# Performance work log

Hardware: AMD Instinct MI355X
Metric: run time of the kernel (lower is better)

## Reference

```python
import jax, jax.numpy as jnp
import numpy as np
from jax import lax

K = 16  # number of KNN neighbors (fixed in module)


def _knn_neighbors(x, k):
    # x: (B, 3, N) point coordinates -> neighbor coords (B, 3, N, K)
    inner = jnp.einsum('bdn,bdm->bnm', x, x)          # (B, N, N)
    sq = jnp.sum(x * x, axis=1)                        # (B, N)
    d2 = sq[:, :, None] + sq[:, None, :] - 2.0 * inner  # pairwise sq dists (B, N, N)
    _, nbr_idx = lax.top_k(-d2, k)                     # k nearest (incl. self), (B, N, K)
    # gather neighbor coordinates: expand x to (B, 3, 1, N), idx to (B, 1, N, K)
    neighbor = jnp.take_along_axis(x[:, :, None, :], nbr_idx[:, None, :, :], axis=3)
    return neighbor  # (B, 3, N, K)


def _down_index(neighbor, x, npts_ds):
    # center-diff saliency: sum of squared offsets to K neighbors per point
    diff = neighbor - x[:, :, :, None]                 # (B, 3, N, K)
    score = jnp.sum(diff * diff, axis=(1, 3))          # (B, N)
    _, idx = lax.top_k(score, npts_ds)                 # (B, npts_ds)
    return idx


def setup_inputs() -> dict:
    key = jax.random.key(0)
    k1, k2 = jax.random.split(key)
    B, N, C = 8, 4096, 128
    x = jax.random.normal(k1, (B, 3, N), dtype=jnp.float32)
    y = jax.random.normal(k2, (B, C, N), dtype=jnp.float32)
    return {"x": x, "y": y, "npts_ds": 2048}


def reference(x, y, npts_ds):
    B, _, N = x.shape
    C = y.shape[1]
    neighbor = _knn_neighbors(x, K)                    # ops.group(x, K, 'neighbor')
    idx = _down_index(neighbor, x, npts_ds)            # ops.down_index(...), (B, npts_ds)
    idx3 = jnp.broadcast_to(idx[:, None, :], (B, 3, npts_ds))
    idxC = jnp.broadcast_to(idx[:, None, :], (B, C, npts_ds))
    top_k_xyz = jnp.take_along_axis(x, idx3, axis=2)    # (B, 3, npts_ds)
    top_k_points = jnp.take_along_axis(y, idxC, axis=2)  # (B, C, npts_ds)
    return (top_k_xyz, top_k_points)
```

## Files before the change

kernel.cpp:

```cpp
#include <hip/hip_runtime.h>
#include <math.h>

#define BATCH 8
#define NPTS 4096
#define CHAN 128
#define KNN 16
#define SPLIT 4
#define CHUNK (NPTS / SPLIT)
#define ISPLIT 2
#define QCH (CHUNK / ISPLIT)
#define EPC 24
#define RSPLIT 4
#define RCHUNK (NPTS / RSPLIT)

typedef unsigned long long u64;

__device__ __forceinline__ u64 pack_key(float d2, int idx) {
  unsigned b = __float_as_uint(d2);
  b ^= (unsigned)((int)b >> 31) | 0x80000000u;
  return ((u64)b << 32) | (unsigned)idx;
}

__device__ __forceinline__ float d2_ref(float4 q, float ppx, float ppy,
                                        float ppz, float psq) {
  float inner = __fadd_rn(__fadd_rn(__fmul_rn(ppx, q.x), __fmul_rn(ppy, q.y)),
                          __fmul_rn(ppz, q.z));
  return __fsub_rn(__fadd_rn(psq, q.w), __fmul_rn(2.0f, inner));
}

__device__ __forceinline__ void ce_asc(u64& x, u64& y) {
  bool sw = y < x;
  u64 lo = sw ? y : x;
  u64 hi = sw ? x : y;
  x = lo;
  y = hi;
}

__device__ __forceinline__ void batcher_sort16_u64(u64 a[16]) {
#define CE(i, j) ce_asc(a[i], a[j])
  CE(0, 8); CE(1, 9); CE(2, 10); CE(3, 11);
  CE(4, 12); CE(5, 13); CE(6, 14); CE(7, 15);
  CE(0, 4); CE(1, 5); CE(2, 6); CE(3, 7);
  CE(8, 12); CE(9, 13); CE(10, 14); CE(11, 15);
  CE(4, 8); CE(5, 9); CE(6, 10); CE(7, 11);
  CE(0, 2); CE(1, 3); CE(4, 6); CE(5, 7);
  CE(8, 10); CE(9, 11); CE(12, 14); CE(13, 15);
  CE(2, 8); CE(3, 9); CE(6, 12); CE(7, 13);
  CE(2, 4); CE(3, 5); CE(6, 8); CE(7, 9); CE(10, 12); CE(11, 13);
  CE(0, 1); CE(2, 3); CE(4, 5); CE(6, 7);
  CE(8, 9); CE(10, 11); CE(12, 13); CE(14, 15);
  CE(1, 8); CE(3, 10); CE(5, 12); CE(7, 14);
  CE(1, 4); CE(3, 6); CE(5, 8); CE(7, 10); CE(9, 12); CE(11, 14);
  CE(1, 2); CE(3, 4); CE(5, 6); CE(7, 8); CE(9, 10); CE(11, 12); CE(13, 14);
#undef CE
}

__device__ __forceinline__ void bitonic_sort32(u64 a[32]) {
#pragma unroll
  for (int k = 2; k <= 32; k <<= 1) {
#pragma unroll
    for (int j = k >> 1; j > 0; j >>= 1) {
#pragma unroll
      for (int i = 0; i < 32; ++i) {
        int l = i ^ j;
        if (l > i) {
          if ((i & k) == 0) ce_asc(a[i], a[l]);
          else              ce_asc(a[l], a[i]);
        }
      }
    }
  }
}

__device__ __forceinline__ void merge_keep16(u64 T[16], const u64 A[16]) {
  u64 nt[16];
#pragma unroll
  for (int i = 0; i < 16; ++i) {
    u64 a = A[15 - i];
    nt[i] = (a < T[i]) ? a : T[i];
  }
#pragma unroll
  for (int j = 8; j > 0; j >>= 1) {
#pragma unroll
    for (int i = 0; i < 16; ++i) {
      int l = i ^ j;
      if (l > i) ce_asc(nt[i], nt[l]);
    }
  }
#pragma unroll
  for (int i = 0; i < 16; ++i) T[i] = nt[i];
}

__device__ __forceinline__ void ce_i32(int& x, int& y) {
  int lo = (x < y) ? x : y;
  int hi = (x < y) ? y : x;
  x = lo;
  y = hi;
}

__device__ __forceinline__ void batcher_sort16_i32(int a[16]) {
#define CE(i, j) ce_i32(a[i], a[j])
  CE(0, 8); CE(1, 9); CE(2, 10); CE(3, 11);
  CE(4, 12); CE(5, 13); CE(6, 14); CE(7, 15);
  CE(0, 4); CE(1, 5); CE(2, 6); CE(3, 7);
  CE(8, 12); CE(9, 13); CE(10, 14); CE(11, 15);
  CE(4, 8); CE(5, 9); CE(6, 10); CE(7, 11);
  CE(0, 2); CE(1, 3); CE(4, 6); CE(5, 7);
  CE(8, 10); CE(9, 11); CE(12, 14); CE(13, 15);
  CE(2, 8); CE(3, 9); CE(6, 12); CE(7, 13);
  CE(2, 4); CE(3, 5); CE(6, 8); CE(7, 9); CE(10, 12); CE(11, 13);
  CE(0, 1); CE(2, 3); CE(4, 5); CE(6, 7);
  CE(8, 9); CE(10, 11); CE(12, 13); CE(14, 15);
  CE(1, 8); CE(3, 10); CE(5, 12); CE(7, 14);
  CE(1, 4); CE(3, 6); CE(5, 8); CE(7, 10); CE(9, 12); CE(11, 14);
  CE(1, 2); CE(3, 4); CE(5, 6); CE(7, 8); CE(9, 10); CE(11, 12); CE(13, 14);
#undef CE
}

__device__ __forceinline__ void merge_keep16_i32(int T[16], const int A[16]) {
  int nt[16];
#pragma unroll
  for (int i = 0; i < 16; ++i) {
    int a = A[15 - i];
    nt[i] = (a < T[i]) ? a : T[i];
  }
#pragma unroll
  for (int j = 8; j > 0; j >>= 1) {
#pragma unroll
    for (int i = 0; i < 16; ++i) {
      int l = i ^ j;
      if (l > i) ce_i32(nt[i], nt[l]);
    }
  }
#pragma unroll
  for (int i = 0; i < 16; ++i) T[i] = nt[i];
}

__global__ __attribute__((amdgpu_waves_per_eu(4, 4)))
__launch_bounds__(512) void knn_partial_kernel(
    const float* __restrict__ x, u64* __restrict__ pkey) {
  const int s = blockIdx.x % SPLIT;
  const int ntile = (blockIdx.x / SPLIT) % (NPTS / 256);
  const int b = blockIdx.x / (SPLIT * (NPTS / 256));
  const int p = threadIdx.x & 255;
  const int h = threadIdx.x >> 8;
  __shared__ float4 xs[CHUNK];
  __shared__ unsigned short ebuf[512 * EPC];
  __shared__ u64 mbuf[KNN][256];

  const float* xb = x + (size_t)b * 3 * NPTS;
  for (int i = threadIdx.x; i < CHUNK; i += 512) {
    int gm = s * CHUNK + i;
    float px = xb[gm];
    float py = xb[NPTS + gm];
    float pz = xb[2 * NPTS + gm];
    float sq = __fadd_rn(__fadd_rn(__fmul_rn(px, px), __fmul_rn(py, py)),
                         __fmul_rn(pz, pz));
    xs[i] = make_float4(px, py, pz, sq);
  }

  const int n = ntile * 256 + p;
  float ppx = xb[n];
  float ppy = xb[NPTS + n];
  float ppz = xb[2 * NPTS + n];
  float psq = __fadd_rn(__fadd_rn(__fmul_rn(ppx, ppx), __fmul_rn(ppy, ppy)),
                        __fmul_rn(ppz, ppz));
  __syncthreads();

  const int cbase = h * QCH;

  int T[16];
#pragma unroll
  for (int i = 0; i < 16; ++i) T[i] = 0x7FFFFFFF;
  int r17 = 0x7FFFFFFF;

#pragma unroll 1
  for (int base = 0; base < QCH; base += 16) {
    int A[16];
#pragma unroll
    for (int t = 0; t < 16; ++t) {
      float4 q = xs[cbase + base + t];
      int bits = __float_as_int(d2_ref(q, ppx, ppy, ppz, psq));
      A[t] = (bits & 0xFFFFFE00) | (base + t);
    }
    batcher_sort16_i32(A);
    int u[16];
#pragma unroll
    for (int i = 0; i < 16; ++i) {
      int a = A[15 - i];
      u[i] = (T[i] < a) ? a : T[i];
    }
#pragma unroll
    for (int w = 8; w > 0; w >>= 1) {
#pragma unroll
      for (int i = 0; i < 16; ++i) {
        if (i < w) u[i] = (u[i] < u[i + w]) ? u[i] : u[i + w];
      }
    }
    r17 = (r17 < u[0]) ? r17 : u[0];
    merge_keep16_i32(T, A);
  }

  const int tau = T[15] & 0xFFFFFE00;
  const bool slow = ((r17 & 0xFFFFFE00) == tau);

  u64 K[16];
  if (!slow) {
#pragma unroll
    for (int j = 0; j < 16; ++j) {
      int loc = cbase + (T[j] & 511);
      float4 q = xs[loc];
      float d2 = d2_ref(q, ppx, ppy, ppz, psq);
      K[j] = pack_key(d2, s * CHUNK + loc);
    }
    batcher_sort16_u64(K);
  } else {
    unsigned short* myb = &ebuf[(unsigned)threadIdx.x * EPC];
    int cnt = 0;
#pragma unroll 4
    for (int m = 0; m < QCH; ++m) {
      float4 q = xs[cbase + m];
      int tb = __float_as_int(d2_ref(q, ppx, ppy, ppz, psq)) & 0xFFFFFE00;
      if (tb <= tau) {
        myb[cnt < EPC - 1 ? cnt : EPC - 1] = (unsigned short)m;
        ++cnt;
      }
    }
    u64 KK[32];
#pragma unroll
    for (int j = 0; j < EPC; ++j) {
      int loc = cbase + (myb[j] & 511);
      float4 q = xs[loc];
      float d2 = d2_ref(q, ppx, ppy, ppz, psq);
      u64 k = pack_key(d2, s * CHUNK + loc);
      KK[j] = (j < cnt) ? k : ~0ull;
    }
#pragma unroll
    for (int j = EPC; j < 32; ++j) KK[j] = ~0ull;
    bitonic_sort32(KK);
#pragma unroll
    for (int j = 0; j < 16; ++j) K[j] = KK[j];
  }

  if (h == 1) {
#pragma unroll
    for (int j = 0; j < 16; ++j) mbuf[j][p] = K[j];
  }
  __syncthreads();
  if (h == 0) {
    u64 A64[16];
#pragma unroll
    for (int j = 0; j < 16; ++j) A64[j] = mbuf[j][p];
    merge_keep16(K, A64);
    u64* pb = pkey + ((size_t)(b * SPLIT + s) * KNN) * NPTS + n;
#pragma unroll
    for (int j = 0; j < 16; ++j) pb[(size_t)j * NPTS] = K[j];
  }
}

__global__ __attribute__((amdgpu_waves_per_eu(1, 2)))
__launch_bounds__(256) void merge_score_kernel(
    const float* __restrict__ x, const u64* __restrict__ pkey,
    float* __restrict__ score, int* __restrict__ cnt) {
  const int b = blockIdx.x / (NPTS / 256);
  const int n = (blockIdx.x % (NPTS / 256)) * 256 + threadIdx.x;

  cnt[(size_t)b * NPTS + n] = 0;

  u64 T[16];
  {
    const u64* pb = pkey + ((size_t)(b * SPLIT + 0) * KNN) * NPTS + n;
#pragma unroll
    for (int j = 0; j < 16; ++j) T[j] = pb[(size_t)j * NPTS];
  }
#pragma unroll
  for (int s = 1; s < SPLIT; ++s) {
    const u64* pb = pkey + ((size_t)(b * SPLIT + s) * KNN) * NPTS + n;
    u64 A[16];
#pragma unroll
    for (int j = 0; j < 16; ++j) A[j] = pb[(size_t)j * NPTS];
    merge_keep16(T, A);
  }

  const float* xb = x + (size_t)b * 3 * NPTS;
  float ppx = xb[n];
  float ppy = xb[NPTS + n];
  float ppz = xb[2 * NPTS + n];

  float nx[KNN], ny[KNN], nz[KNN];
#pragma unroll
  for (int j = 0; j < KNN; ++j) {
    int idx = (int)(unsigned)T[j];
    nx[j] = xb[idx];
    ny[j] = xb[NPTS + idx];
    nz[j] = xb[2 * NPTS + idx];
  }

  float P[3];
#pragma unroll
  for (int d = 0; d < 3; ++d) {
    const float pc = (d == 0) ? ppx : ((d == 1) ? ppy : ppz);
    float r[8];
#pragma unroll
    for (int j = 0; j < 8; ++j) {
      float c0 = (d == 0) ? nx[j] : ((d == 1) ? ny[j] : nz[j]);
      float c1 = (d == 0) ? nx[j + 8] : ((d == 1) ? ny[j + 8] : nz[j + 8]);
      float e0 = __fsub_rn(c0, pc);
      float e1 = __fsub_rn(c1, pc);
      r[j] = __fadd_rn(__fmul_rn(e0, e0), __fmul_rn(e1, e1));
    }
    float t0 = __fadd_rn(r[0], r[1]);
    float t1 = __fadd_rn(r[2], r[3]);
    float t2 = __fadd_rn(r[4], r[5]);
    float t3 = __fadd_rn(r[6], r[7]);
    P[d] = __fadd_rn(__fadd_rn(t0, t1), __fadd_rn(t2, t3));
  }
  score[(size_t)b * NPTS + n] =
      __fadd_rn(__fadd_rn(P[0], P[1]), P[2]);
}

__global__ __launch_bounds__(256) void rank_partial_kernel(
    const float* __restrict__ score, int* __restrict__ cnt) {
  const int s = blockIdx.x % RSPLIT;
  const int ntile = (blockIdx.x / RSPLIT) % (NPTS / 256);
  const int b = blockIdx.x / (RSPLIT * (NPTS / 256));
  __shared__ float ss[RCHUNK];

  const float* sb = score + (size_t)b * NPTS;
  for (int i = threadIdx.x; i < RCHUNK; i += 256)
    ss[i] = sb[s * RCHUNK + i];

  const int n = ntile * 256 + threadIdx.x;
  const float sn = sb[n];
  __syncthreads();

  int c = 0;
#pragma unroll 8
  for (int mm = 0; mm < RCHUNK; ++mm) {
    float sm = ss[mm];
    int gm = s * RCHUNK + mm;
    c += (sm > sn) || (sm == sn && gm < n);
  }
  atomicAdd(&cnt[(size_t)b * NPTS + n], c);
}

__global__ __launch_bounds__(256) void rank_scatter_kernel(
    const int* __restrict__ cnt, int* __restrict__ sel, int npts) {
  int t = blockIdx.x * 256 + threadIdx.x;
  int b = t / NPTS;
  int n = t % NPTS;
  int c = cnt[t];
  if (c < npts) sel[(size_t)b * npts + c] = n;
}

__global__ __launch_bounds__(256) void gather_kernel(
    const float* __restrict__ x, const float* __restrict__ y,
    const int* __restrict__ sel, float* __restrict__ out, int npts,
    int total0, int total) {
  int tid = blockIdx.x * blockDim.x + threadIdx.x;
  if (tid >= total) return;
  if (tid < total0) {
    int j = tid % npts;
    int rest = tid / npts;
    int d = rest % 3;
    int b = rest / 3;
    int src = sel[b * npts + j];
    out[tid] = x[((size_t)b * 3 + d) * NPTS + src];
  } else {
    int t = tid - total0;
    int j = t % npts;
    int rest = t / npts;
    int c = rest % CHAN;
    int b = rest / CHAN;
    int src = sel[b * npts + j];
    out[tid] = y[((size_t)b * CHAN + c) * NPTS + src];
  }
}

extern "C" void kernel_launch(void* const* d_in, const int* in_sizes, int n_in,
                              void* d_out, int out_size, void* d_ws,
                              size_t ws_size, hipStream_t stream) {
  const float* x = (const float*)d_in[0];
  const float* y = (const float*)d_in[1];
  float* out = (float*)d_out;

  const int npts = out_size / (BATCH * (3 + CHAN));

  char* w = (char*)d_ws;
  u64* pkey = (u64*)w;
  w += sizeof(u64) * (size_t)BATCH * SPLIT * KNN * NPTS;
  float* score = (float*)w;
  w += sizeof(float) * (size_t)BATCH * NPTS;
  int* cnt = (int*)w;
  w += sizeof(int) * (size_t)BATCH * NPTS;
  int* sel = (int*)w;

  knn_partial_kernel<<<BATCH * (NPTS / 256) * SPLIT, 512, 0, stream>>>(
      x, pkey);
  merge_score_kernel<<<BATCH * NPTS / 256, 256, 0, stream>>>(x, pkey, score,
                                                             cnt);
  rank_partial_kernel<<<BATCH * (NPTS / 256) * RSPLIT, 256, 0, stream>>>(
      score, cnt);
  rank_scatter_kernel<<<BATCH * NPTS / 256, 256, 0, stream>>>(cnt, sel, npts);

  const int total0 = BATCH * 3 * npts;
  gather_kernel<<<(out_size + 255) / 256, 256, 0, stream>>>(
      x, y, sel, out, npts, total0, out_size);
}
```

Before: 256.0 us.

## Split KNN candidate scan four ways per query tile with serial LDS merge

Each block now covers 128 query points instead of 256, and each query's candidate chunk is split across four thread groups instead of two, so the grid doubles and the per-thread scan gets shorter. The index field packed into the sort key shrinks from 9 to 8 bits, which keeps one more bit of distance precision in the approximate key. The four partial top-16 lists are merged in three serialized rounds through one shared buffer that replaces the old ebuf/mbuf pair. The cost is more syncthreads, idle threads during the merges, and the shared point chunk being loaded twice as often overall.

Result: faster. 249.5 us (-2.5%).

```diff
diff --git a/kernel.cpp b/kernel.cpp
--- a/kernel.cpp
+++ b/kernel.cpp
@@ -7,8 +7,9 @@
 #define KNN 16
 #define SPLIT 4
 #define CHUNK (NPTS / SPLIT)
-#define ISPLIT 2
+#define ISPLIT 4
 #define QCH (CHUNK / ISPLIT)
+#define PTILE 128
 #define EPC 24
 #define RSPLIT 4
 #define RCHUNK (NPTS / RSPLIT)
@@ -140,13 +141,12 @@
 __launch_bounds__(512) void knn_partial_kernel(
     const float* __restrict__ x, u64* __restrict__ pkey) {
   const int s = blockIdx.x % SPLIT;
-  const int ntile = (blockIdx.x / SPLIT) % (NPTS / 256);
-  const int b = blockIdx.x / (SPLIT * (NPTS / 256));
-  const int p = threadIdx.x & 255;
-  const int h = threadIdx.x >> 8;
+  const int ntile = (blockIdx.x / SPLIT) % (NPTS / PTILE);
+  const int b = blockIdx.x / (SPLIT * (NPTS / PTILE));
+  const int p = threadIdx.x & (PTILE - 1);
+  const int q4 = threadIdx.x >> 7;
   __shared__ float4 xs[CHUNK];
-  __shared__ unsigned short ebuf[512 * EPC];
-  __shared__ u64 mbuf[KNN][256];
+  __shared__ u64 ubuf[3072];
 
   const float* xb = x + (size_t)b * 3 * NPTS;
   for (int i = threadIdx.x; i < CHUNK; i += 512) {
@@ -159,7 +159,7 @@
     xs[i] = make_float4(px, py, pz, sq);
   }
 
-  const int n = ntile * 256 + p;
+  const int n = ntile * PTILE + p;
   float ppx = xb[n];
   float ppy = xb[NPTS + n];
   float ppz = xb[2 * NPTS + n];
@@ -167,7 +167,7 @@
                         __fmul_rn(ppz, ppz));
   __syncthreads();
 
-  const int cbase = h * QCH;
+  const int cbase = q4 * QCH;
 
   int T[16];
 #pragma unroll
@@ -181,7 +181,7 @@
     for (int t = 0; t < 16; ++t) {
       float4 q = xs[cbase + base + t];
       int bits = __float_as_int(d2_ref(q, ppx, ppy, ppz, psq));
-      A[t] = (bits & 0xFFFFFE00) | (base + t);
+      A[t] = (bits & 0xFFFFFF00) | (base + t);
     }
     batcher_sort16_i32(A);
     int u[16];
@@ -201,26 +201,27 @@
     merge_keep16_i32(T, A);
   }
 
-  const int tau = T[15] & 0xFFFFFE00;
-  const bool slow = ((r17 & 0xFFFFFE00) == tau);
+  const int tau = T[15] & 0xFFFFFF00;
+  const bool slow = ((r17 & 0xFFFFFF00) == tau);
 
   u64 K[16];
   if (!slow) {
 #pragma unroll
     for (int j = 0; j < 16; ++j) {
-      int loc = cbase + (T[j] & 511);
+      int loc = cbase + (T[j] & 255);
       float4 q = xs[loc];
       float d2 = d2_ref(q, ppx, ppy, ppz, psq);
       K[j] = pack_key(d2, s * CHUNK + loc);
     }
     batcher_sort16_u64(K);
   } else {
-    unsigned short* myb = &ebuf[(unsigned)threadIdx.x * EPC];
+    unsigned short* myb =
+        reinterpret_cast<unsigned short*>(ubuf) + (unsigned)threadIdx.x * EPC;
     int cnt = 0;
 #pragma unroll 4
     for (int m = 0; m < QCH; ++m) {
       float4 q = xs[cbase + m];
-      int tb = __float_as_int(d2_ref(q, ppx, ppy, ppz, psq)) & 0xFFFFFE00;
+      int tb = __float_as_int(d2_ref(q, ppx, ppy, ppz, psq)) & 0xFFFFFF00;
       if (tb <= tau) {
         myb[cnt < EPC - 1 ? cnt : EPC - 1] = (unsigned short)m;
         ++cnt;
@@ -229,7 +230,7 @@
     u64 KK[32];
 #pragma unroll
     for (int j = 0; j < EPC; ++j) {
-      int loc = cbase + (myb[j] & 511);
+      int loc = cbase + (myb[j] & (QCH - 1));
       float4 q = xs[loc];
       float d2 = d2_ref(q, ppx, ppy, ppz, psq);
       u64 k = pack_key(d2, s * CHUNK + loc);
@@ -242,16 +243,24 @@
     for (int j = 0; j < 16; ++j) K[j] = KK[j];
   }
 
-  if (h == 1) {
-#pragma unroll
-    for (int j = 0; j < 16; ++j) mbuf[j][p] = K[j];
-  }
   __syncthreads();
-  if (h == 0) {
-    u64 A64[16];
-#pragma unroll
-    for (int j = 0; j < 16; ++j) A64[j] = mbuf[j][p];
-    merge_keep16(K, A64);
+  u64(*L)[PTILE] = reinterpret_cast<u64(*)[PTILE]>(ubuf);
+#pragma unroll 1
+  for (int r = 1; r <= 3; ++r) {
+    if (q4 == r) {
+#pragma unroll
+      for (int j = 0; j < 16; ++j) L[j][p] = K[j];
+    }
+    __syncthreads();
+    if (q4 == 0) {
+      u64 A64[16];
+#pragma unroll
+      for (int j = 0; j < 16; ++j) A64[j] = L[j][p];
+      merge_keep16(K, A64);
+    }
+    __syncthreads();
+  }
+  if (q4 == 0) {
     u64* pb = pkey + ((size_t)(b * SPLIT + s) * KNN) * NPTS + n;
 #pragma unroll
     for (int j = 0; j < 16; ++j) pb[(size_t)j * NPTS] = K[j];
@@ -395,7 +404,7 @@
   w += sizeof(int) * (size_t)BATCH * NPTS;
   int* sel = (int*)w;
 
-  knn_partial_kernel<<<BATCH * (NPTS / 256) * SPLIT, 512, 0, stream>>>(
+  knn_partial_kernel<<<BATCH * (NPTS / PTILE) * SPLIT, 512, 0, stream>>>(
       x, pkey);
   merge_score_kernel<<<BATCH * NPTS / 256, 256, 0, stream>>>(x, pkey, score,
                                                              cnt);
```
